# Kernel tuning notes

Measured on AMD Instinct MI355X. Metric: run time of the kernel, lower is better.

Reference implementation:

```python
import jax, jax.numpy as jnp
import numpy as np

B, N, C, P, K = 8, 65536, 96, 96, 512


def _ln(x, g, b, eps=1e-5):
    mu = x.mean(axis=-1, keepdims=True)
    var = ((x - mu) ** 2).mean(axis=-1, keepdims=True)
    return (x - mu) * jax.lax.rsqrt(var + eps) * g + b


def setup_inputs():
    key = jax.random.key(0)
    ks = jax.random.split(key, 8)
    inp = {
        "pts_feat": jax.random.normal(ks[0], (B, N, C), jnp.float32),
        "sp_idx": jax.random.randint(ks[1], (B, N), 0, K, jnp.int64),
        "all_xyz": jax.random.normal(ks[2], (B, N, 3), jnp.float32),
        # pts_proj1: Linear(3,P) -> LN -> ReLU -> Linear(P,P) -> LN
        "W1": jax.random.normal(ks[3], (3, P), jnp.float32) / np.sqrt(3.0),
        "b1": jnp.zeros((P,), jnp.float32),
        "g1": jnp.ones((P,), jnp.float32),
        "be1": jnp.zeros((P,), jnp.float32),
        "W2": jax.random.normal(ks[4], (P, P), jnp.float32) / np.sqrt(P),
        "b2": jnp.zeros((P,), jnp.float32),
        "g2": jnp.ones((P,), jnp.float32),
        "be2": jnp.zeros((P,), jnp.float32),
        # pts_proj2: Linear(2P,P) -> LN -> ReLU -> Linear(P,1,no bias) -> Sigmoid
        "W3": jax.random.normal(ks[5], (2 * P, P), jnp.float32) / np.sqrt(2.0 * P),
        "b3": jnp.zeros((P,), jnp.float32),
        "g3": jnp.ones((P,), jnp.float32),
        "be3": jnp.zeros((P,), jnp.float32),
        "W4": jax.random.normal(ks[6], (P, 1), jnp.float32) / np.sqrt(P),
        "num_sp": K,
    }
    return inp


def reference(pts_feat, sp_idx, all_xyz, W1, b1, g1, be1, W2, b2, g2, be2,
              W3, b3, g3, be3, W4, num_sp):
    Bx, Nx, Cx = pts_feat.shape
    S = Bx * num_sp  # total superpoints across batch (uniform K per batch)
    idx = (sp_idx + jnp.arange(Bx, dtype=sp_idx.dtype)[:, None] * num_sp).reshape(-1)
    xyz = all_xyz.reshape(-1, 3)
    feat = pts_feat.reshape(-1, Cx)

    # scatter_norm: unit-sphere normalize per segment
    mn = jax.ops.segment_min(xyz, idx, num_segments=S)
    mx = jax.ops.segment_max(xyz, idx, num_segments=S)
    cnt = jax.ops.segment_sum(jnp.ones((xyz.shape[0],), xyz.dtype), idx, num_segments=S)
    cnt_c = jnp.maximum(cnt, 1.0)
    center = jax.ops.segment_sum(xyz, idx, num_segments=S) / cnt_c[:, None]
    diam = (mx - mn).max(axis=1)
    pts = (xyz - center[idx]) / (diam[idx][:, None] + 0.01)

    # pts_proj1
    h = _ln(pts @ W1 + b1, g1, be1)
    h = jax.nn.relu(h)
    h = _ln(h @ W2 + b2, g2, be2)

    seg = jax.ops.segment_max(h, idx, num_segments=S)  # (S, P)
    cat = jnp.concatenate([h, seg[idx]], axis=-1)      # (B*N, 2P)

    # pts_proj2
    z = _ln(cat @ W3 + b3, g3, be3)
    z = jax.nn.relu(z)
    w = jax.nn.sigmoid(z @ W4) * 2.0                   # (B*N, 1)

    sp_feat = jax.ops.segment_sum(feat * w, idx, num_segments=S) / cnt_c[:, None] + seg
    return sp_feat.reshape(Bx, num_sp, Cx), w.reshape(Bx, Nx, 1)
```

## Files before the change

kernel.cpp:

```cpp
#include <hip/hip_runtime.h>
#include <cstdint>

#define MM 524288
#define NSEG 4096

#define WS_SCNT   0u
#define WS_CURSOR 4096u
#define WS_OFFS   8192u
#define WS_M1     12288u
#define WS_SEGF   28688u
#define WS_ZSEG   421904u
#define WS_SORTED 815120u
#define WS_SEG16  1339408u
#define WS_WSRT   1601552u
#define WS_H8     2125840u
#define WS_PTS    27291664u
#define WS_END    28864528u

typedef __attribute__((ext_vector_type(8))) short short8;
typedef __attribute__((ext_vector_type(4))) float f32x4;

#define WPAD 104

__device__ __forceinline__ unsigned bfr(float x) {
    unsigned u = __float_as_uint(x);
    return (u + 0x7FFFu + ((u >> 16) & 1u)) >> 16;
}
__device__ __forceinline__ float bf2f(unsigned v) {
    return __uint_as_float(v << 16);
}
union U4S8 { uint4 u; short8 s; };

__global__ void __launch_bounds__(256) k0_init(unsigned* __restrict__ ws)
{
    unsigned i = blockIdx.x * 256u + threadIdx.x;
    if (i < 8192u) ws[i] = 0u;
}

__global__ void __launch_bounds__(256) k1_count(
    const int* __restrict__ spidx, unsigned* __restrict__ scnt)
{
    __shared__ unsigned lcnt[512];
    int tid = threadIdx.x;
    for (int j = tid; j < 512; j += 256) lcnt[j] = 0u;
    __syncthreads();
    int base = blockIdx.x * 4096;
    #pragma unroll 4
    for (int it = 0; it < 16; ++it) {
        int p = base + it*256 + tid;
        atomicAdd(&lcnt[spidx[p]], 1u);
    }
    __syncthreads();
    int b = blockIdx.x >> 4;
    for (int j = tid; j < 512; j += 256)
        atomicAdd(&scnt[(b << 9) + j], lcnt[j]);
}

__global__ void __launch_bounds__(1024) k2_scan(
    const unsigned* __restrict__ scnt, unsigned* __restrict__ offs,
    const float* __restrict__ W1, const float* __restrict__ b1, float* __restrict__ m1)
{
    __shared__ unsigned sh[1024];
    int t = threadIdx.x;
    unsigned c0 = scnt[t*4+0], c1 = scnt[t*4+1], c2 = scnt[t*4+2], c3 = scnt[t*4+3];
    unsigned tot = c0 + c1 + c2 + c3;
    sh[t] = tot;
    __syncthreads();
    for (int d = 1; d < 1024; d <<= 1) {
        unsigned v = (t >= d) ? sh[t-d] : 0u;
        __syncthreads();
        sh[t] += v;
        __syncthreads();
    }
    unsigned excl = sh[t] - tot;
    offs[t*4+0] = excl;
    offs[t*4+1] = excl + c0;
    offs[t*4+2] = excl + c0 + c1;
    offs[t*4+3] = excl + c0 + c1 + c2;

    if (t == 0) {
        float Sa=0,Sb=0,Sc=0,Sd=0,Saa=0,Sbb=0,Scc=0,Sdd=0,Sab=0,Sac=0,Sad=0,Sbc=0,Sbd=0,Scd=0;
        #pragma unroll 8
        for (int j = 0; j < 96; ++j) {
            float A = W1[j], B2 = W1[96+j], C2 = W1[192+j], D = b1[j];
            Sa+=A; Sb+=B2; Sc+=C2; Sd+=D;
            Saa=fmaf(A,A,Saa); Sbb=fmaf(B2,B2,Sbb); Scc=fmaf(C2,C2,Scc); Sdd=fmaf(D,D,Sdd);
            Sab=fmaf(A,B2,Sab); Sac=fmaf(A,C2,Sac); Sad=fmaf(A,D,Sad);
            Sbc=fmaf(B2,C2,Sbc); Sbd=fmaf(B2,D,Sbd); Scd=fmaf(C2,D,Scd);
        }
        const float inv = 1.f/96.f;
        float Am=Sa*inv, Bm=Sb*inv, Cm=Sc*inv, Dm=Sd*inv;
        m1[0]=Am; m1[1]=Bm; m1[2]=Cm; m1[3]=Dm;
        m1[4]=Saa*inv-Am*Am; m1[5]=Sbb*inv-Bm*Bm; m1[6]=Scc*inv-Cm*Cm; m1[7]=Sdd*inv-Dm*Dm;
        m1[8]=Sab*inv-Am*Bm; m1[9]=Sac*inv-Am*Cm; m1[10]=Sad*inv-Am*Dm;
        m1[11]=Sbc*inv-Bm*Cm; m1[12]=Sbd*inv-Bm*Dm; m1[13]=Scd*inv-Cm*Dm;
    }
}

__global__ void __launch_bounds__(256) k3_scatter(
    const int* __restrict__ spidx, const unsigned* __restrict__ offs,
    unsigned* __restrict__ cursor, unsigned* __restrict__ sorted,
    unsigned short* __restrict__ seg16)
{
    __shared__ unsigned lcnt[512];
    __shared__ unsigned gbase[512];
    __shared__ unsigned short rank16[4096];
    int tid = threadIdx.x;
    for (int j = tid; j < 512; j += 256) lcnt[j] = 0u;
    __syncthreads();
    int base = blockIdx.x * 4096;
    #pragma unroll 4
    for (int it = 0; it < 16; ++it) {
        int p = base + it*256 + tid;
        unsigned r = atomicAdd(&lcnt[spidx[p]], 1u);
        rank16[it*256 + tid] = (unsigned short)r;
    }
    __syncthreads();
    int b = blockIdx.x >> 4;
    for (int j = tid; j < 512; j += 256)
        gbase[j] = atomicAdd(&cursor[(b << 9) + j], lcnt[j]);
    __syncthreads();
    #pragma unroll 4
    for (int it = 0; it < 16; ++it) {
        int p = base + it*256 + tid;
        int sl = spidx[p];
        int s = (b << 9) + sl;
        unsigned pos = offs[s] + gbase[sl] + (unsigned)rank16[it*256 + tid];
        sorted[pos] = (unsigned)p;
        seg16[pos] = (unsigned short)s;
    }
}

__global__ void __launch_bounds__(128) k3b_stats(
    const float* __restrict__ xyz, const unsigned* __restrict__ sorted,
    const unsigned* __restrict__ offs, const unsigned* __restrict__ scnt,
    float* __restrict__ pts)
{
    int s = blockIdx.x, tid = threadIdx.x;
    unsigned cnt = scnt[s], off = offs[s];
    float mnx=INFINITY, mny=INFINITY, mnz=INFINITY;
    float mxx=-INFINITY, mxy=-INFINITY, mxz=-INFINITY;
    float smx=0.f, smy=0.f, smz=0.f;
    for (unsigned r = tid; r < cnt; r += 128) {
        unsigned p = sorted[off + r];
        float x = xyz[3*p], y = xyz[3*p+1], z = xyz[3*p+2];
        mnx = fminf(mnx, x); mny = fminf(mny, y); mnz = fminf(mnz, z);
        mxx = fmaxf(mxx, x); mxy = fmaxf(mxy, y); mxz = fmaxf(mxz, z);
        smx += x; smy += y; smz += z;
    }
    #pragma unroll
    for (int m = 1; m < 64; m <<= 1) {
        mnx = fminf(mnx, __shfl_xor(mnx, m)); mny = fminf(mny, __shfl_xor(mny, m));
        mnz = fminf(mnz, __shfl_xor(mnz, m));
        mxx = fmaxf(mxx, __shfl_xor(mxx, m)); mxy = fmaxf(mxy, __shfl_xor(mxy, m));
        mxz = fmaxf(mxz, __shfl_xor(mxz, m));
        smx += __shfl_xor(smx, m); smy += __shfl_xor(smy, m); smz += __shfl_xor(smz, m);
    }
    __shared__ float cw[2][9];
    __shared__ float cd[4];
    if ((tid & 63) == 0) {
        int w = tid >> 6;
        cw[w][0]=mnx; cw[w][1]=mny; cw[w][2]=mnz;
        cw[w][3]=mxx; cw[w][4]=mxy; cw[w][5]=mxz;
        cw[w][6]=smx; cw[w][7]=smy; cw[w][8]=smz;
    }
    __syncthreads();
    if (tid == 0) {
        float a0=fminf(cw[0][0],cw[1][0]), a1=fminf(cw[0][1],cw[1][1]), a2=fminf(cw[0][2],cw[1][2]);
        float b0=fmaxf(cw[0][3],cw[1][3]), b1=fmaxf(cw[0][4],cw[1][4]), b2=fmaxf(cw[0][5],cw[1][5]);
        float s0=cw[0][6]+cw[1][6], s1=cw[0][7]+cw[1][7], s2=cw[0][8]+cw[1][8];
        float cc = fmaxf((float)cnt, 1.f);
        float dm = fmaxf(fmaxf(b0-a0, b1-a1), b2-a2);
        cd[0] = s0/cc; cd[1] = s1/cc; cd[2] = s2/cc;
        cd[3] = 1.f / (dm + 0.01f);
    }
    __syncthreads();
    float cx = cd[0], cy = cd[1], cz = cd[2], dinv = cd[3];
    for (unsigned r = tid; r < cnt; r += 128) {
        unsigned p = sorted[off + r];
        unsigned o = off + r;
        pts[o]              = (xyz[3*p+0] - cx) * dinv;
        pts[MM + o]         = (xyz[3*p+1] - cy) * dinv;
        pts[2u*MM + o]      = (xyz[3*p+2] - cz) * dinv;
    }
}

__global__ void __launch_bounds__(256) kTA(
    const float* __restrict__ pts,
    const float* __restrict__ W1, const float* __restrict__ b1,
    const float* __restrict__ g1, const float* __restrict__ be1,
    const float* __restrict__ m1,
    const float* __restrict__ W2, const float* __restrict__ b2,
    const float* __restrict__ g2, const float* __restrict__ be2,
    uint4* __restrict__ h8)
{
    __shared__ unsigned short wT[96*WPAD];
    __shared__ float pw8[96*8];
    __shared__ float prm[3*96];
    __shared__ float mcl[14];
    int tid = threadIdx.x;
    #pragma unroll 4
    for (int it = 0; it < 36; ++it) {
        int e = it*256 + tid;
        int i = e / 96, j = e - i*96;
        wT[j*WPAD + i] = (unsigned short)bfr(W2[e]);
    }
    if (tid < 96) {
        pw8[tid*8+0] = W1[tid]; pw8[tid*8+1] = W1[96+tid]; pw8[tid*8+2] = W1[192+tid];
        pw8[tid*8+3] = b1[tid]; pw8[tid*8+4] = g1[tid];    pw8[tid*8+5] = be1[tid];
        pw8[tid*8+6] = 0.f;     pw8[tid*8+7] = 0.f;
        prm[tid] = b2[tid]; prm[96+tid] = g2[tid]; prm[192+tid] = be2[tid];
    }
    if (tid < 14) mcl[tid] = m1[tid];
    __syncthreads();

    int lane = tid & 63, w = tid >> 6;
    int pcol = lane & 15, g = lane >> 4;
    size_t slot0 = (size_t)blockIdx.x * 256 + w*64 + pcol;
    const f32x4* pwv = (const f32x4*)pw8;

    #pragma unroll 1
    for (int t = 0; t < 4; ++t) {
        size_t slot = slot0 + (size_t)t * 16;
        float px = pts[slot];
        float py = pts[(size_t)MM + slot];
        float pz = pts[2u*(size_t)MM + slot];

        float mu = fmaf(px, mcl[0], fmaf(py, mcl[1], fmaf(pz, mcl[2], mcl[3])));
        float var = fmaf(px*px, mcl[4], fmaf(py*py, mcl[5], fmaf(pz*pz, mcl[6], mcl[7])));
        var = fmaf(2.f*px*py, mcl[8],  var);
        var = fmaf(2.f*px*pz, mcl[9],  var);
        var = fmaf(2.f*px,    mcl[10], var);
        var = fmaf(2.f*py*pz, mcl[11], var);
        var = fmaf(2.f*py,    mcl[12], var);
        var = fmaf(2.f*pz,    mcl[13], var);
        float rs = rsqrtf(var + 1e-5f);

        f32x4 acc[6];
        #pragma unroll
        for (int nt = 0; nt < 6; ++nt) acc[nt] = (f32x4){0.f,0.f,0.f,0.f};

        #pragma unroll
        for (int ks = 0; ks < 3; ++ks) {
            U4S8 bu;
            unsigned vv[4];
            #pragma unroll
            for (int e2 = 0; e2 < 4; ++e2) {
                int i0 = ks*32 + g*8 + e2*2;
                f32x4 lo0 = pwv[i0*2],     hi0 = pwv[i0*2+1];
                f32x4 lo1 = pwv[(i0+1)*2], hi1 = pwv[(i0+1)*2+1];
                float ta = fmaf(px, lo0[0], fmaf(py, lo0[1], fmaf(pz, lo0[2], lo0[3])));
                ta = fmaxf(fmaf((ta - mu) * rs, hi0[0], hi0[1]), 0.f);
                float tb = fmaf(px, lo1[0], fmaf(py, lo1[1], fmaf(pz, lo1[2], lo1[3])));
                tb = fmaxf(fmaf((tb - mu) * rs, hi1[0], hi1[1]), 0.f);
                vv[e2] = bfr(ta) | (bfr(tb) << 16);
            }
            bu.u.x = vv[0]; bu.u.y = vv[1]; bu.u.z = vv[2]; bu.u.w = vv[3];
            #pragma unroll
            for (int nt = 0; nt < 6; ++nt) {
                const short8 aF = *(const short8*)&wT[(nt*16 + pcol)*WPAD + ks*32 + g*8];
                acc[nt] = __builtin_amdgcn_mfma_f32_16x16x32_bf16(aF, bu.s, acc[nt], 0, 0, 0);
            }
        }

        float sum = 0.f, sq = 0.f;
        #pragma unroll
        for (int nt = 0; nt < 6; ++nt) {
            f32x4 bv = *(const f32x4*)&prm[nt*16 + g*4];
            #pragma unroll
            for (int r = 0; r < 4; ++r) {
                float v = acc[nt][r] + bv[r];
                acc[nt][r] = v;
                sum += v;
                sq = fmaf(v, v, sq);
            }
        }
        sum += __shfl_xor(sum, 16); sum += __shfl_xor(sum, 32);
        sq  += __shfl_xor(sq, 16);  sq  += __shfl_xor(sq, 32);
        float muh = sum * (1.f/96.f);
        float rsh = rsqrtf(sq * (1.f/96.f) - muh*muh + 1e-5f);

        #pragma unroll
        for (int nt = 0; nt < 6; ++nt) {
            f32x4 gv  = *(const f32x4*)&prm[96  + nt*16 + g*4];
            f32x4 bev = *(const f32x4*)&prm[192 + nt*16 + g*4];
            float o0 = fmaf((acc[nt][0]-muh)*rsh, gv[0], bev[0]);
            float o1 = fmaf((acc[nt][1]-muh)*rsh, gv[1], bev[1]);
            float o2 = fmaf((acc[nt][2]-muh)*rsh, gv[2], bev[2]);
            float o3 = fmaf((acc[nt][3]-muh)*rsh, gv[3], bev[3]);
            uint2 st;
            st.x = bfr(o0) | (bfr(o1) << 16);
            st.y = bfr(o2) | (bfr(o3) << 16);
            int j0 = nt*16 + g*4;
            size_t q = (size_t)(nt*2 + (g >> 1));
            *(uint2*)((char*)h8 + (q*MM + slot)*16 + (size_t)(j0 & 7)*2) = st;
        }
    }
}

__global__ void __launch_bounds__(192) kB_seg(
    const uint4* __restrict__ h8,
    const unsigned* __restrict__ offs, const unsigned* __restrict__ scnt,
    const float* __restrict__ W3, const float* __restrict__ b3,
    float* __restrict__ segf, float* __restrict__ zseg)
{
    __shared__ uint4 st[2][16][13];
    __shared__ float lseg[96];
    int s = blockIdx.x, tid = threadIdx.x;
    unsigned cnt = scnt[s], off = offs[s];
    int r = tid & 15, q = tid >> 4;
    float mx = -INFINITY;

    if (q < 12) {
        uint4 v = make_uint4(0xFF80FF80u, 0xFF80FF80u, 0xFF80FF80u, 0xFF80FF80u);
        if ((unsigned)r < cnt) v = h8[(size_t)q * MM + off + r];
        st[0][r][q] = v;
    }
    __syncthreads();

    for (unsigned base = 0; base < cnt; base += 16) {
        int cur = (int)((base >> 4) & 1u);
        unsigned nb = base + 16;
        if (nb < cnt && q < 12) {
            uint4 v = make_uint4(0xFF80FF80u, 0xFF80FF80u, 0xFF80FF80u, 0xFF80FF80u);
            if (nb + (unsigned)r < cnt) v = h8[(size_t)q * MM + off + nb + r];
            st[cur ^ 1][r][q] = v;
        }
        if (tid < 96) {
            int qj = tid >> 3, ej = tid & 7;
            #pragma unroll
            for (int rr = 0; rr < 16; ++rr) {
                const unsigned short* hp = (const unsigned short*)&st[cur][rr][qj];
                mx = fmaxf(mx, bf2f(hp[ej]));
            }
        }
        __syncthreads();
    }
    if (tid < 96) { segf[(size_t)s*96 + tid] = mx; lseg[tid] = mx; }
    __syncthreads();
    if (tid < 96) {
        float acc = b3[tid];
        #pragma unroll 4
        for (int i = 0; i < 96; ++i)
            acc = fmaf(lseg[i], W3[(size_t)(96+i)*96 + tid], acc);
        zseg[(size_t)s*96 + tid] = acc;
    }
}

__global__ void __launch_bounds__(256) kC_mfma(
    const uint4* __restrict__ h8, const float* __restrict__ zseg,
    const unsigned short* __restrict__ seg16, const unsigned* __restrict__ sorted,
    const float* __restrict__ W3, const float* __restrict__ g3,
    const float* __restrict__ be3, const float* __restrict__ W4,
    float* __restrict__ w_nat, float* __restrict__ w_srt)
{
    __shared__ unsigned short wT[96*WPAD];
    __shared__ float prm[3*96];
    int tid = threadIdx.x;
    #pragma unroll 4
    for (int it = 0; it < 36; ++it) {
        int e = it*256 + tid;
        int i = e / 96, j = e - i*96;
        wT[j*WPAD + i] = (unsigned short)bfr(W3[e]);
    }
    if (tid < 96) { prm[tid] = g3[tid]; prm[96+tid] = be3[tid]; prm[192+tid] = W4[tid]; }
    __syncthreads();

    int lane = tid & 63, w = tid >> 6;
    int pcol = lane & 15, g = lane >> 4;
    size_t slot0 = (size_t)blockIdx.x * 256 + w*64 + pcol;

    uint4 B0 = h8[(size_t)(0*4+g) * MM + slot0];
    uint4 B1 = h8[(size_t)(1*4+g) * MM + slot0];
    uint4 B2q = h8[(size_t)(2*4+g) * MM + slot0];

    #pragma unroll 1
    for (int t = 0; t < 4; ++t) {
        size_t slot = slot0 + (size_t)t * 16;
        uint4 C0 = B0, C1 = B1, C2 = B2q;
        if (t < 3) {
            size_t sn = slot + 16;
            C0 = h8[(size_t)(0*4+g) * MM + sn];
            C1 = h8[(size_t)(1*4+g) * MM + sn];
            C2 = h8[(size_t)(2*4+g) * MM + sn];
        }
        U4S8 u0, u1, u2; u0.u = B0; u1.u = B1; u2.u = B2q;
        short8 bB[3] = { u0.s, u1.s, u2.s };

        f32x4 acc[6];
        #pragma unroll
        for (int nt = 0; nt < 6; ++nt) acc[nt] = (f32x4){0.f,0.f,0.f,0.f};

        #pragma unroll
        for (int ks = 0; ks < 3; ++ks) {
            #pragma unroll
            for (int nt = 0; nt < 6; ++nt) {
                const short8 aF = *(const short8*)&wT[(nt*16 + pcol)*WPAD + ks*32 + g*8];
                acc[nt] = __builtin_amdgcn_mfma_f32_16x16x32_bf16(aF, bB[ks], acc[nt], 0, 0, 0);
            }
        }

        int s = seg16[slot];
        float sum = 0.f, sq = 0.f;
        #pragma unroll
        for (int nt = 0; nt < 6; ++nt) {
            f32x4 zs = *(const f32x4*)&zseg[(size_t)s*96 + nt*16 + g*4];
            #pragma unroll
            for (int r = 0; r < 4; ++r) {
                float v = acc[nt][r] + zs[r];
                acc[nt][r] = v;
                sum += v;
                sq = fmaf(v, v, sq);
            }
        }
        sum += __shfl_xor(sum, 16); sum += __shfl_xor(sum, 32);
        sq  += __shfl_xor(sq, 16);  sq  += __shfl_xor(sq, 32);
        float mu = sum * (1.f/96.f);
        float rs = rsqrtf(sq * (1.f/96.f) - mu*mu + 1e-5f);

        float tt = 0.f;
        #pragma unroll
        for (int nt = 0; nt < 6; ++nt) {
            f32x4 gv  = *(const f32x4*)&prm[nt*16 + g*4];
            f32x4 bev = *(const f32x4*)&prm[96 + nt*16 + g*4];
            f32x4 w4v = *(const f32x4*)&prm[192 + nt*16 + g*4];
            #pragma unroll
            for (int r = 0; r < 4; ++r) {
                float v = fmaxf(fmaf((acc[nt][r]-mu)*rs, gv[r], bev[r]), 0.f);
                tt = fmaf(v, w4v[r], tt);
            }
        }
        tt += __shfl_xor(tt, 16); tt += __shfl_xor(tt, 32);
        if (lane < 16) {
            float wv = 2.f / (1.f + expf(-tt));
            w_srt[slot] = wv;
            w_nat[sorted[slot]] = wv;
        }
        B0 = C0; B1 = C1; B2q = C2;
    }
}

__global__ void __launch_bounds__(128) kD_pool(
    const float* __restrict__ feat, const float* __restrict__ w_srt,
    const unsigned* __restrict__ sorted, const unsigned* __restrict__ offs,
    const unsigned* __restrict__ scnt, const float* __restrict__ segf,
    float* __restrict__ sp_out)
{
    int s = blockIdx.x;
    int c = threadIdx.x;
    unsigned cnt = scnt[s], off = offs[s];
    float acc = 0.f;
    unsigned r = 0;
    for (; r + 16 <= cnt; r += 16) {
        unsigned pp[16]; float ww[16];
        #pragma unroll
        for (int k = 0; k < 16; ++k) {
            pp[k] = sorted[off + r + k];
            ww[k] = w_srt[off + r + k];
        }
        if (c < 96) {
            #pragma unroll
            for (int k = 0; k < 16; ++k)
                acc = fmaf(feat[(size_t)pp[k]*96 + c], ww[k], acc);
        }
    }
    for (; r + 4 <= cnt; r += 4) {
        unsigned pp[4]; float ww[4];
        #pragma unroll
        for (int k = 0; k < 4; ++k) {
            pp[k] = sorted[off + r + k];
            ww[k] = w_srt[off + r + k];
        }
        if (c < 96) {
            #pragma unroll
            for (int k = 0; k < 4; ++k)
                acc = fmaf(feat[(size_t)pp[k]*96 + c], ww[k], acc);
        }
    }
    for (; r < cnt; ++r) {
        unsigned p0 = sorted[off + r];
        float w0 = w_srt[off + r];
        if (c < 96) acc = fmaf(feat[(size_t)p0*96 + c], w0, acc);
    }
    if (c < 96) {
        float cc = fmaxf((float)cnt, 1.f);
        sp_out[(size_t)s*96 + c] = acc / cc + segf[(size_t)s*96 + c];
    }
}

extern "C" void kernel_launch(void* const* d_in, const int* in_sizes, int n_in,
                              void* d_out, int out_size, void* d_ws, size_t ws_size,
                              hipStream_t stream)
{
    const float* pts_feat = (const float*)d_in[0];
    const int*   sp_idx   = (const int*)d_in[1];
    const float* xyz      = (const float*)d_in[2];
    const float* W1  = (const float*)d_in[3];
    const float* b1  = (const float*)d_in[4];
    const float* g1  = (const float*)d_in[5];
    const float* be1 = (const float*)d_in[6];
    const float* W2  = (const float*)d_in[7];
    const float* b2  = (const float*)d_in[8];
    const float* g2  = (const float*)d_in[9];
    const float* be2 = (const float*)d_in[10];
    const float* W3  = (const float*)d_in[11];
    const float* b3  = (const float*)d_in[12];
    const float* g3  = (const float*)d_in[13];
    const float* be3 = (const float*)d_in[14];
    const float* W4  = (const float*)d_in[15];

    float* out = (float*)d_out;
    float* sp_out = out;
    float* w_out  = out + (size_t)NSEG * 96;

    if (ws_size < (size_t)WS_END * 4u) return;

    unsigned* ws32   = (unsigned*)d_ws;
    unsigned* scnt   = ws32 + WS_SCNT;
    unsigned* cursor = ws32 + WS_CURSOR;
    unsigned* offs   = ws32 + WS_OFFS;
    float*    m1     = (float*)(ws32 + WS_M1);
    float*    segf   = (float*)(ws32 + WS_SEGF);
    float*    zseg   = (float*)(ws32 + WS_ZSEG);
    unsigned* sorted = ws32 + WS_SORTED;
    unsigned short* seg16 = (unsigned short*)(ws32 + WS_SEG16);
    float*    w_srt  = (float*)(ws32 + WS_WSRT);
    uint4*    h8     = (uint4*)(ws32 + WS_H8);
    float*    pts    = (float*)(ws32 + WS_PTS);

    k0_init<<<32, 256, 0, stream>>>(ws32);
    k1_count<<<MM/4096, 256, 0, stream>>>(sp_idx, scnt);
    k2_scan<<<1, 1024, 0, stream>>>(scnt, offs, W1, b1, m1);
    k3_scatter<<<MM/4096, 256, 0, stream>>>(sp_idx, offs, cursor, sorted, seg16);
    k3b_stats<<<NSEG, 128, 0, stream>>>(xyz, sorted, offs, scnt, pts);
    kTA<<<MM/256, 256, 0, stream>>>(pts, W1, b1, g1, be1, m1,
        W2, b2, g2, be2, h8);
    kB_seg<<<NSEG, 192, 0, stream>>>(h8, offs, scnt, W3, b3, segf, zseg);
    kC_mfma<<<MM/256, 256, 0, stream>>>(h8, zseg, seg16, sorted, W3, g3, be3, W4,
        w_out, w_srt);
    kD_pool<<<NSEG, 128, 0, stream>>>(pts_feat, w_srt, sorted, offs, scnt, segf, sp_out);
}
```

Baseline: 264.5 us.

## Recompute pts_proj1 in the final MLP kernel instead of reloading stored h

```diff
diff --git a/kernel.cpp b/kernel.cpp
--- a/kernel.cpp
+++ b/kernel.cpp
@@ -347,45 +347,65 @@
     }
 }
 
-__global__ void __launch_bounds__(256) kC_mfma(
-    const uint4* __restrict__ h8, const float* __restrict__ zseg,
+__global__ void __launch_bounds__(256) kC_rec(
+    const float* __restrict__ pts, const float* __restrict__ zseg,
     const unsigned short* __restrict__ seg16, const unsigned* __restrict__ sorted,
+    const float* __restrict__ W1, const float* __restrict__ b1,
+    const float* __restrict__ g1, const float* __restrict__ be1,
+    const float* __restrict__ m1,
+    const float* __restrict__ W2, const float* __restrict__ b2,
+    const float* __restrict__ g2, const float* __restrict__ be2,
     const float* __restrict__ W3, const float* __restrict__ g3,
     const float* __restrict__ be3, const float* __restrict__ W4,
     float* __restrict__ w_nat, float* __restrict__ w_srt)
 {
-    __shared__ unsigned short wT[96*WPAD];
-    __shared__ float prm[3*96];
+    __shared__ unsigned short wT2[96*WPAD];
+    __shared__ unsigned short wT3[96*WPAD];
+    __shared__ float pw8[96*8];
+    __shared__ float prm2[3*96];
+    __shared__ float prm3[3*96];
+    __shared__ float mcl[14];
+    __shared__ __align__(16) unsigned short tbuf[4][16*104];
     int tid = threadIdx.x;
     #pragma unroll 4
     for (int it = 0; it < 36; ++it) {
         int e = it*256 + tid;
         int i = e / 96, j = e - i*96;
-        wT[j*WPAD + i] = (unsigned short)bfr(W3[e]);
-    }
-    if (tid < 96) { prm[tid] = g3[tid]; prm[96+tid] = be3[tid]; prm[192+tid] = W4[tid]; }
+        wT2[j*WPAD + i] = (unsigned short)bfr(W2[e]);
+        wT3[j*WPAD + i] = (unsigned short)bfr(W3[e]);
+    }
+    if (tid < 96) {
+        pw8[tid*8+0] = W1[tid]; pw8[tid*8+1] = W1[96+tid]; pw8[tid*8+2] = W1[192+tid];
+        pw8[tid*8+3] = b1[tid]; pw8[tid*8+4] = g1[tid];    pw8[tid*8+5] = be1[tid];
+        pw8[tid*8+6] = 0.f;     pw8[tid*8+7] = 0.f;
+        prm2[tid] = b2[tid]; prm2[96+tid] = g2[tid]; prm2[192+tid] = be2[tid];
+        prm3[tid] = g3[tid]; prm3[96+tid] = be3[tid]; prm3[192+tid] = W4[tid];
+    }
+    if (tid < 14) mcl[tid] = m1[tid];
     __syncthreads();
 
     int lane = tid & 63, w = tid >> 6;
     int pcol = lane & 15, g = lane >> 4;
     size_t slot0 = (size_t)blockIdx.x * 256 + w*64 + pcol;
-
-    uint4 B0 = h8[(size_t)(0*4+g) * MM + slot0];
-    uint4 B1 = h8[(size_t)(1*4+g) * MM + slot0];
-    uint4 B2q = h8[(size_t)(2*4+g) * MM + slot0];
+    const f32x4* pwv = (const f32x4*)pw8;
+    unsigned short* tb = &tbuf[w][0];
 
     #pragma unroll 1
     for (int t = 0; t < 4; ++t) {
         size_t slot = slot0 + (size_t)t * 16;
-        uint4 C0 = B0, C1 = B1, C2 = B2q;
-        if (t < 3) {
-            size_t sn = slot + 16;
-            C0 = h8[(size_t)(0*4+g) * MM + sn];
-            C1 = h8[(size_t)(1*4+g) * MM + sn];
-            C2 = h8[(size_t)(2*4+g) * MM + sn];
-        }
-        U4S8 u0, u1, u2; u0.u = B0; u1.u = B1; u2.u = B2q;
-        short8 bB[3] = { u0.s, u1.s, u2.s };
+        float px = pts[slot];
+        float py = pts[(size_t)MM + slot];
+        float pz = pts[2u*(size_t)MM + slot];
+
+        float mu = fmaf(px, mcl[0], fmaf(py, mcl[1], fmaf(pz, mcl[2], mcl[3])));
+        float var = fmaf(px*px, mcl[4], fmaf(py*py, mcl[5], fmaf(pz*pz, mcl[6], mcl[7])));
+        var = fmaf(2.f*px*py, mcl[8],  var);
+        var = fmaf(2.f*px*pz, mcl[9],  var);
+        var = fmaf(2.f*px,    mcl[10], var);
+        var = fmaf(2.f*py*pz, mcl[11], var);
+        var = fmaf(2.f*py,    mcl[12], var);
+        var = fmaf(2.f*pz,    mcl[13], var);
+        float rs = rsqrtf(var + 1e-5f);
 
         f32x4 acc[6];
         #pragma unroll
@@ -393,21 +413,34 @@
 
         #pragma unroll
         for (int ks = 0; ks < 3; ++ks) {
+            U4S8 bu;
+            unsigned vv[4];
+            #pragma unroll
+            for (int e2 = 0; e2 < 4; ++e2) {
+                int i0 = ks*32 + g*8 + e2*2;
+                f32x4 lo0 = pwv[i0*2],     hi0 = pwv[i0*2+1];
+                f32x4 lo1 = pwv[(i0+1)*2], hi1 = pwv[(i0+1)*2+1];
+                float ta = fmaf(px, lo0[0], fmaf(py, lo0[1], fmaf(pz, lo0[2], lo0[3])));
+                ta = fmaxf(fmaf((ta - mu) * rs, hi0[0], hi0[1]), 0.f);
+                float tb2 = fmaf(px, lo1[0], fmaf(py, lo1[1], fmaf(pz, lo1[2], lo1[3])));
+                tb2 = fmaxf(fmaf((tb2 - mu) * rs, hi1[0], hi1[1]), 0.f);
+                vv[e2] = bfr(ta) | (bfr(tb2) << 16);
+            }
+            bu.u.x = vv[0]; bu.u.y = vv[1]; bu.u.z = vv[2]; bu.u.w = vv[3];
             #pragma unroll
             for (int nt = 0; nt < 6; ++nt) {
-                const short8 aF = *(const short8*)&wT[(nt*16 + pcol)*WPAD + ks*32 + g*8];
-                acc[nt] = __builtin_amdgcn_mfma_f32_16x16x32_bf16(aF, bB[ks], acc[nt], 0, 0, 0);
-            }
-        }
-
-        int s = seg16[slot];
+                const short8 aF = *(const short8*)&wT2[(nt*16 + pcol)*WPAD + ks*32 + g*8];
+                acc[nt] = __builtin_amdgcn_mfma_f32_16x16x32_bf16(aF, bu.s, acc[nt], 0, 0, 0);
+            }
+        }
+
         float sum = 0.f, sq = 0.f;
         #pragma unroll
         for (int nt = 0; nt < 6; ++nt) {
-            f32x4 zs = *(const f32x4*)&zseg[(size_t)s*96 + nt*16 + g*4];
+            f32x4 bv = *(const f32x4*)&prm2[nt*16 + g*4];
             #pragma unroll
             for (int r = 0; r < 4; ++r) {
-                float v = acc[nt][r] + zs[r];
+                float v = acc[nt][r] + bv[r];
                 acc[nt][r] = v;
                 sum += v;
                 sq = fmaf(v, v, sq);
@@ -415,18 +448,66 @@
         }
         sum += __shfl_xor(sum, 16); sum += __shfl_xor(sum, 32);
         sq  += __shfl_xor(sq, 16);  sq  += __shfl_xor(sq, 32);
-        float mu = sum * (1.f/96.f);
-        float rs = rsqrtf(sq * (1.f/96.f) - mu*mu + 1e-5f);
+        float muh = sum * (1.f/96.f);
+        float rsh = rsqrtf(sq * (1.f/96.f) - muh*muh + 1e-5f);
+
+        #pragma unroll
+        for (int nt = 0; nt < 6; ++nt) {
+            f32x4 gv  = *(const f32x4*)&prm2[96  + nt*16 + g*4];
+            f32x4 bev = *(const f32x4*)&prm2[192 + nt*16 + g*4];
+            float o0 = fmaf((acc[nt][0]-muh)*rsh, gv[0], bev[0]);
+            float o1 = fmaf((acc[nt][1]-muh)*rsh, gv[1], bev[1]);
+            float o2 = fmaf((acc[nt][2]-muh)*rsh, gv[2], bev[2]);
+            float o3 = fmaf((acc[nt][3]-muh)*rsh, gv[3], bev[3]);
+            uint2 st;
+            st.x = bfr(o0) | (bfr(o1) << 16);
+            st.y = bfr(o2) | (bfr(o3) << 16);
+            *(uint2*)&tb[pcol*104 + nt*16 + g*4] = st;
+        }
+        U4S8 hb[3];
+        #pragma unroll
+        for (int ks = 0; ks < 3; ++ks)
+            hb[ks].u = *(const uint4*)&tb[pcol*104 + ks*32 + g*8];
+
+        f32x4 a2[6];
+        #pragma unroll
+        for (int nt = 0; nt < 6; ++nt) a2[nt] = (f32x4){0.f,0.f,0.f,0.f};
+        #pragma unroll
+        for (int ks = 0; ks < 3; ++ks) {
+            #pragma unroll
+            for (int nt = 0; nt < 6; ++nt) {
+                const short8 aF = *(const short8*)&wT3[(nt*16 + pcol)*WPAD + ks*32 + g*8];
+                a2[nt] = __builtin_amdgcn_mfma_f32_16x16x32_bf16(aF, hb[ks].s, a2[nt], 0, 0, 0);
+            }
+        }
+
+        int s = seg16[slot];
+        float sum3 = 0.f, sq3 = 0.f;
+        #pragma unroll
+        for (int nt = 0; nt < 6; ++nt) {
+            f32x4 zs = *(const f32x4*)&zseg[(size_t)s*96 + nt*16 + g*4];
+            #pragma unroll
+            for (int r = 0; r < 4; ++r) {
+                float v = a2[nt][r] + zs[r];
+                a2[nt][r] = v;
+                sum3 += v;
+                sq3 = fmaf(v, v, sq3);
+            }
+        }
+        sum3 += __shfl_xor(sum3, 16); sum3 += __shfl_xor(sum3, 32);
+        sq3  += __shfl_xor(sq3, 16);  sq3  += __shfl_xor(sq3, 32);
+        float mu3 = sum3 * (1.f/96.f);
+        float rs3 = rsqrtf(sq3 * (1.f/96.f) - mu3*mu3 + 1e-5f);
 
         float tt = 0.f;
         #pragma unroll
         for (int nt = 0; nt < 6; ++nt) {
-            f32x4 gv  = *(const f32x4*)&prm[nt*16 + g*4];
-            f32x4 bev = *(const f32x4*)&prm[96 + nt*16 + g*4];
-            f32x4 w4v = *(const f32x4*)&prm[192 + nt*16 + g*4];
+            f32x4 gv  = *(const f32x4*)&prm3[nt*16 + g*4];
+            f32x4 bev = *(const f32x4*)&prm3[96 + nt*16 + g*4];
+            f32x4 w4v = *(const f32x4*)&prm3[192 + nt*16 + g*4];
             #pragma unroll
             for (int r = 0; r < 4; ++r) {
-                float v = fmaxf(fmaf((acc[nt][r]-mu)*rs, gv[r], bev[r]), 0.f);
+                float v = fmaxf(fmaf((a2[nt][r]-mu3)*rs3, gv[r], bev[r]), 0.f);
                 tt = fmaf(v, w4v[r], tt);
             }
         }
@@ -436,7 +517,6 @@
             w_srt[slot] = wv;
             w_nat[sorted[slot]] = wv;
         }
-        B0 = C0; B1 = C1; B2q = C2;
     }
 }
 
@@ -536,7 +616,7 @@
     kTA<<<MM/256, 256, 0, stream>>>(pts, W1, b1, g1, be1, m1,
         W2, b2, g2, be2, h8);
     kB_seg<<<NSEG, 192, 0, stream>>>(h8, offs, scnt, W3, b3, segf, zseg);
-    kC_mfma<<<MM/256, 256, 0, stream>>>(h8, zseg, seg16, sorted, W3, g3, be3, W4,
-        w_out, w_srt);
+    kC_rec<<<MM/256, 256, 0, stream>>>(pts, zseg, seg16, sorted,
+        W1, b1, g1, be1, m1, W2, b2, g2, be2, W3, g3, be3, W4, w_out, w_srt);
     kD_pool<<<NSEG, 128, 0, stream>>>(pts_feat, w_srt, sorted, offs, scnt, segf, sp_out);
 }
```

After: 355.3 us. +34.3%, slower.
